# Performance work log

Measured on AMD Instinct MI355X. Metric: run time of the kernel, lower is better.

Reference implementation:

```python
import jax, jax.numpy as jnp
import numpy as np

B, L, D = 2, 256, 256  # batch, length, raw feature dim (W dims are D+1)

def setup_inputs() -> dict:
    key = jax.random.key(0)
    k1, k2, k3, kw = jax.random.split(key, 4)
    layer1 = jax.random.normal(k1, (B, L, D), dtype=jnp.float32)
    layer2 = jax.random.normal(k2, (B, L, D), dtype=jnp.float32)
    layer3 = jax.random.normal(k3, (B, L, D), dtype=jnp.float32)
    # xavier_normal_ for a 3D tensor: fan_in = D+1 * (D+1) receptive? torch treats
    # dim0 as fan_out-ish; we just use a matched-scale gaussian (correctness of the
    # contraction math is what matters for the kernel baseline).
    std = float(np.sqrt(2.0 / ((D + 1) + (D + 1) * (D + 1))))
    W = jax.random.normal(kw, (D + 1, D + 1, D + 1), dtype=jnp.float32) * std
    return {"layer1": layer1, "layer2": layer2, "layer3": layer3, "W": W}

def _append_ones(x):
    ones = jnp.ones(x.shape[:2] + (1,), dtype=x.dtype)
    return jnp.concatenate([x, ones], axis=-1)

def reference(layer1, layer2, layer3, W):
    l1 = _append_ones(layer1)  # [n, L, a]
    l2 = _append_ones(layer2)  # [n, L, b]
    l3 = _append_ones(layer3)  # [n, L, c]
    # Chained contraction: nia,abc -> nibc ; nibc,njb -> nijc ; nijc,nkc -> nijk
    t = jnp.einsum('nia,abc->nibc', l1, W)
    t = jnp.einsum('nibc,njb->nijc', t, l2)
    out = jnp.einsum('nijc,nkc->nijk', t, l3)
    return out
```

## Files before the change

### kernel.cpp

```cpp
#include <hip/hip_runtime.h>

typedef unsigned short u16;
typedef __attribute__((ext_vector_type(8))) short bf16x8;
typedef __attribute__((ext_vector_type(4))) float f32x4;

#define GLOAD_LDS16(gsrc, ldst)                                               \
  __builtin_amdgcn_global_load_lds(                                           \
      (const __attribute__((address_space(1))) void*)(gsrc),                  \
      (__attribute__((address_space(3))) void*)(ldst), 16, 0, 0)

#define LDSOFF(p) \
  ((unsigned)(uintptr_t)(__attribute__((address_space(3))) const void*)(p))

#define SB0 __builtin_amdgcn_sched_barrier(0)

__device__ __forceinline__ u16 f2bf(float x) {
  unsigned u = __float_as_uint(x);
  u = (u + 0x7FFFu + ((u >> 16) & 1u)) >> 16;
  return (u16)u;
}

__global__ void prep_l_kernel(const float* __restrict__ l1,
                              const float* __restrict__ l2,
                              const float* __restrict__ l3,
                              u16* __restrict__ o1, u16* __restrict__ o2,
                              u16* __restrict__ o3) {
  int idx = blockIdx.x * 256 + threadIdx.x;
  const int NR = 512 * 288;
  if (idx >= 3 * NR) return;
  int which = idx / NR, rem = idx - which * NR;
  int r = rem / 288, p = rem - r * 288;
  const float* s = which == 0 ? l1 : which == 1 ? l2 : l3;
  u16* d = which == 0 ? o1 : which == 1 ? o2 : o3;
  float v = (p < 256) ? s[r * 256 + p] : (p == 256 ? 1.0f : 0.0f);
  d[rem] = f2bf(v);
}

__global__ __launch_bounds__(256, 4) void prep_w_kernel(
    const float* __restrict__ W, u16* __restrict__ W2) {
  __shared__ float tf[64][65];
  const int a0 = blockIdx.x * 64, c0 = blockIdx.y * 64, b = blockIdx.z;
  const int t = threadIdx.x;
  const bool bok = (b < 257);

  float v[16];
#pragma unroll
  for (int i = 0; i < 16; ++i) {
    int idx = t + i * 256;
    int ar = idx >> 6, cc = idx & 63;
    int a = a0 + ar, c = c0 + cc;
    v[i] = (bok && a < 257 && c < 257) ? W[((long)a * 257 + b) * 257 + c] : 0.0f;
  }
#pragma unroll
  for (int i = 0; i < 16; ++i) {
    int idx = t + i * 256;
    int ar = idx >> 6, cc = idx & 63;
    tf[cc][ar] = v[i];
  }
  __syncthreads();

#pragma unroll
  for (int p = 0; p < 2; ++p) {
    int q = t + p * 256;
    int cr = q >> 3, ach = q & 7;
    int c = c0 + cr;
    int abase = a0 + ach * 8;
    if (c < 288 && abase < 288) {
      u16 pk[8];
#pragma unroll
      for (int j = 0; j < 8; ++j) pk[j] = f2bf(tf[cr][ach * 8 + j]);
      *(uint4*)(&W2[((long)c * 288 + b) * 288 + abase]) = *(uint4*)pk;
    }
  }
}

__global__ __launch_bounds__(256, 3) void gemm_nt(
    const u16* __restrict__ A, const u16* __restrict__ B, u16* __restrict__ C,
    int K, int lda, int ldb, int ldc) {
  __shared__ u16 As[2][4096];
  __shared__ u16 Bs[2][4096];
  const int t = threadIdx.x;
  const int bid = blockIdx.x;
  const int xcd = bid & 7, s = bid >> 3;
  const int nt = xcd * 77 + (s >> 2);
  const int mt = s & 3;
  const int m0 = mt * 128, n0 = nt * 128;
  const int lane = t & 63;
  const int w = t >> 6;
  const int wr = (w >> 1) * 64, wc = (w & 1) * 64;
  const int r16 = lane & 15;
  const int cgrp = lane >> 4;
  const int rr = cgrp * 4;
  const unsigned ABase = LDSOFF(&As[0][0]);
  const unsigned BBase = LDSOFF(&Bs[0][0]);
  (void)K;

  const u16* PA = A + (long)m0 * lda;
  const u16* PB = B + (long)n0 * ldb;

#define STG(buf, k0)                                                          \
  {                                                                           \
    _Pragma("unroll") for (int _p = 0; _p < 2; ++_p) {                        \
      int _q = t + _p * 256;                                                  \
      int _r = _q >> 2, _g = (_q & 3) ^ ((_r >> 1) & 3);                      \
      GLOAD_LDS16(PA + (long)_r * lda + (k0) + _g * 8, &As[buf][_q * 8]);     \
      GLOAD_LDS16(PB + (long)_r * ldb + (k0) + _g * 8, &Bs[buf][_q * 8]);     \
    }                                                                         \
  }

  f32x4 acc[4][4];
  const f32x4 zero = {0.f, 0.f, 0.f, 0.f};
#pragma unroll
  for (int i = 0; i < 4; ++i)
#pragma unroll
    for (int j = 0; j < 4; ++j) acc[i][j] = zero;

  STG(0, 0);

#define GCOL(NI)                                                              \
  __builtin_amdgcn_s_setprio(1);                                              \
  _Pragma("unroll") for (int _mi = 0; _mi < 4; ++_mi)                         \
    acc[_mi][NI] = __builtin_amdgcn_mfma_f32_16x16x32_bf16(                   \
        af[_mi], bf[NI], acc[_mi][NI], 0, 0, 0);                              \
  __builtin_amdgcn_s_setprio(0);                                              \
  SB0;

#define GSTEP(KS)                                                             \
  {                                                                           \
    asm volatile("s_waitcnt vmcnt(0)" ::: "memory");                          \
    SB0;                                                                      \
    __builtin_amdgcn_s_barrier();                                             \
    SB0;                                                                      \
    bf16x8 af[4], bf[4];                                                      \
    _Pragma("unroll") for (int mi = 0; mi < 4; ++mi) {                        \
      int R = wr + mi * 16 + r16;                                             \
      unsigned ao = ABase + (unsigned)(((((KS) & 1) * 4096) + R * 32 +        \
                                       ((cgrp ^ ((R >> 1) & 3)) * 8)) * 2);   \
      asm volatile("ds_read_b128 %0, %1" : "=v"(af[mi]) : "v"(ao));           \
    }                                                                         \
    _Pragma("unroll") for (int ni = 0; ni < 4; ++ni) {                        \
      int R = wc + ni * 16 + r16;                                             \
      unsigned ao = BBase + (unsigned)(((((KS) & 1) * 4096) + R * 32 +        \
                                       ((cgrp ^ ((R >> 1) & 3)) * 8)) * 2);   \
      asm volatile("ds_read_b128 %0, %1" : "=v"(bf[ni]) : "v"(ao));           \
    }                                                                         \
    SB0;                                                                      \
    if ((KS) < 8) STG(((KS) + 1) & 1, ((KS) + 1) * 32);                       \
    SB0;                                                                      \
    asm volatile("s_waitcnt lgkmcnt(3)" ::: "memory"); SB0;                   \
    GCOL(0)                                                                   \
    asm volatile("s_waitcnt lgkmcnt(2)" ::: "memory"); SB0;                   \
    GCOL(1)                                                                   \
    asm volatile("s_waitcnt lgkmcnt(1)" ::: "memory"); SB0;                   \
    GCOL(2)                                                                   \
    asm volatile("s_waitcnt lgkmcnt(0)" ::: "memory"); SB0;                   \
    GCOL(3)                                                                   \
  }

  GSTEP(0) GSTEP(1) GSTEP(2) GSTEP(3) GSTEP(4)
  GSTEP(5) GSTEP(6) GSTEP(7) GSTEP(8)
#undef GSTEP
#undef GCOL
#undef STG

#pragma unroll
  for (int mi = 0; mi < 4; ++mi) {
    int gm = m0 + wr + mi * 16 + rr;
#pragma unroll
    for (int ni = 0; ni < 4; ++ni) {
      int gc = n0 + wc + ni * 16 + r16;
#pragma unroll
      for (int r = 0; r < 4; ++r)
        C[(long)(gm + r) * ldc + gc] = f2bf(acc[mi][ni][r]);
    }
  }
}

__global__ __launch_bounds__(512, 4) void fused23(
    const u16* __restrict__ l2b, const u16* __restrict__ l3b,
    const u16* __restrict__ T1, float* __restrict__ out) {
  __shared__ u16 S[64 * 280];
  __shared__ u16 Bst[2][8704];
  const int t = threadIdx.x;
  const int lane = t & 63;
  const int w = t >> 6;

  const int bid = blockIdx.x;
  const int xcd = bid & 7;
  const int seq = bid >> 3;
  const int ni = xcd * 64 + (seq >> 2);
  const int q = seq & 3;
  const int n = ni >> 8;

  const int r16 = lane & 15;
  const int cgrp = lane >> 4;
  const int kb = cgrp * 8;
  const int rr = cgrp * 4;
  const f32x4 zero = {0.f, 0.f, 0.f, 0.f};

  const u16* A2 = l2b + (long)n * 73728 + (long)(q * 64) * 288;
  const u16* BT = T1 + (long)ni * 82944;
  const u16* B3 = l3b + (long)n * 73728;
  const unsigned BOF = LDSOFF(&Bst[0][0]);
  const unsigned SOF = LDSOFF(&S[0]);

#define ISSUE_A(buf, kk)                                                      \
  {                                                                           \
    int _q1 = w * 136 + lane;                                                 \
    int _r1 = _q1 >> 2, _g1 = (_q1 & 3) ^ ((_r1 >> 1) & 3);                   \
    GLOAD_LDS16(BT + (long)_r1 * 288 + (kk) * 32 + _g1 * 8,                   \
                &Bst[(buf)][_q1 * 8]);                                        \
    int _q2 = _q1 + 64;                                                       \
    int _r2 = _q2 >> 2, _g2 = (_q2 & 3) ^ ((_r2 >> 1) & 3);                   \
    GLOAD_LDS16(BT + (long)_r2 * 288 + (kk) * 32 + _g2 * 8,                   \
                &Bst[(buf)][_q2 * 8]);                                        \
    if (lane < 8) {                                                           \
      int _q3 = w * 136 + 128 + lane;                                         \
      int _r3 = _q3 >> 2, _g3 = (_q3 & 3) ^ ((_r3 >> 1) & 3);                 \
      GLOAD_LDS16(BT + (long)_r3 * 288 + (kk) * 32 + _g3 * 8,                 \
                  &Bst[(buf)][_q3 * 8]);                                      \
    }                                                                         \
  }
#define ISSUE_B(buf, kk)                                                      \
  {                                                                           \
    _Pragma("unroll") for (int _p = 0; _p < 2; ++_p) {                        \
      int _q = w * 128 + lane + _p * 64;                                      \
      int _r = _q >> 2, _g = (_q & 3) ^ ((_r >> 1) & 3);                      \
      GLOAD_LDS16(B3 + (long)_r * 288 + (kk) * 32 + _g * 8,                   \
                  &Bst[(buf)][_q * 8]);                                       \
    }                                                                         \
  }

  {
    const int wjA = w & 1, wcA = w >> 1;
    const int NT = (wcA == 3) ? 5 : 4;
    f32x4 acc[2][5];
#pragma unroll
    for (int i = 0; i < 2; ++i)
#pragma unroll
      for (int j = 0; j < 5; ++j) acc[i][j] = zero;

    const u16* Ap = A2 + (long)(wjA * 32 + r16) * 288 + kb;
    bf16x8 afc0 = *(const bf16x8*)(Ap);
    bf16x8 afc1 = *(const bf16x8*)(Ap + 16 * 288);
    bf16x8 afn0, afn1;
    SB0;
    ISSUE_A(0, 0) SB0;
    ISSUE_A(1, 1) SB0;

#define FA_STEP(K)                                                            \
  {                                                                           \
    asm volatile("s_waitcnt vmcnt(0)" ::: "memory");                          \
    SB0;                                                                      \
    __builtin_amdgcn_s_barrier();                                             \
    SB0;                                                                      \
    bf16x8 bf[5];                                                             \
    _Pragma("unroll") for (int i = 0; i < 5; ++i) if (i < NT) {               \
      const int R = wcA * 64 + i * 16 + r16;                                  \
      unsigned ao = BOF + (unsigned)((((K) & 1) * 8704 + R * 32 +             \
                                      ((cgrp ^ ((R >> 1) & 3)) * 8)) * 2);    \
      asm volatile("ds_read_b128 %0, %1" : "=v"(bf[i]) : "v"(ao));            \
    }                                                                         \
    SB0;                                                                      \
    if ((K) < 8) {                                                            \
      ISSUE_A(((K) + 1) & 1, (K) + 1);                                        \
      afn0 = *(const bf16x8*)(Ap + ((K) + 1) * 32);                           \
      afn1 = *(const bf16x8*)(Ap + 16 * 288 + ((K) + 1) * 32);                \
    }                                                                         \
    SB0;                                                                      \
    asm volatile("s_waitcnt lgkmcnt(0)" ::: "memory");                        \
    SB0;                                                                      \
    __builtin_amdgcn_s_setprio(1);                                            \
    _Pragma("unroll") for (int i = 0; i < 5; ++i) if (i < NT) {               \
      acc[0][i] = __builtin_amdgcn_mfma_f32_16x16x32_bf16(                    \
          afc0, bf[i], acc[0][i], 0, 0, 0);                                   \
      acc[1][i] = __builtin_amdgcn_mfma_f32_16x16x32_bf16(                    \
          afc1, bf[i], acc[1][i], 0, 0, 0);                                   \
    }                                                                         \
    __builtin_amdgcn_s_setprio(0);                                            \
    SB0;                                                                      \
    afc0 = afn0; afc1 = afn1;                                                 \
  }
    FA_STEP(0) FA_STEP(1) FA_STEP(2) FA_STEP(3) FA_STEP(4)
    FA_STEP(5) FA_STEP(6) FA_STEP(7) FA_STEP(8)
#undef FA_STEP

    __syncthreads();
    ISSUE_B(0, 0);
#pragma unroll
    for (int i = 0; i < 5; ++i) if (i < NT)
#pragma unroll
      for (int mi = 0; mi < 2; ++mi)
#pragma unroll
        for (int qq = 0; qq < 4; ++qq)
          S[(wjA * 32 + mi * 16 + rr + qq) * 280 + wcA * 64 + i * 16 + r16] =
              f2bf(acc[mi][i][qq]);
  }
  __syncthreads();

  {
    const int wjb = w & 1, wk = w >> 1;
    f32x4 acc[2][4];
#pragma unroll
    for (int i = 0; i < 2; ++i)
#pragma unroll
      for (int j = 0; j < 4; ++j) acc[i][j] = zero;

#define FB_MM(NI)                                                             \
  __builtin_amdgcn_s_setprio(1);                                              \
  acc[0][NI] = __builtin_amdgcn_mfma_f32_16x16x32_bf16(af[0], bf[NI], acc[0][NI], 0, 0, 0); \
  acc[1][NI] = __builtin_amdgcn_mfma_f32_16x16x32_bf16(af[1], bf[NI], acc[1][NI], 0, 0, 0); \
  __builtin_amdgcn_s_setprio(0);                                              \
  SB0;

#define FB_STEP(K)                                                            \
  {                                                                           \
    asm volatile("s_waitcnt vmcnt(0)" ::: "memory");                          \
    SB0;                                                                      \
    __builtin_amdgcn_s_barrier();                                             \
    SB0;                                                                      \
    bf16x8 af[2], bf[4];                                                      \
    _Pragma("unroll") for (int mi = 0; mi < 2; ++mi) {                        \
      unsigned ao = SOF + (unsigned)(((wjb * 32 + mi * 16 + r16) * 280 +      \
                                      (K) * 32 + kb) * 2);                    \
      asm volatile("ds_read_b128 %0, %1" : "=v"(af[mi]) : "v"(ao));           \
    }                                                                         \
    _Pragma("unroll") for (int nj = 0; nj < 4; ++nj) {                        \
      const int R = wk * 64 + nj * 16 + r16;                                  \
      unsigned ao = BOF + (unsigned)((((K) & 1) * 8704 + R * 32 +             \
                                      ((cgrp ^ ((R >> 1) & 3)) * 8)) * 2);    \
      asm volatile("ds_read_b128 %0, %1" : "=v"(bf[nj]) : "v"(ao));           \
    }                                                                         \
    SB0;                                                                      \
    if ((K) < 7) ISSUE_B(((K) + 1) & 1, (K) + 1);                             \
    SB0;                                                                      \
    asm volatile("s_waitcnt lgkmcnt(3)" ::: "memory"); SB0;                   \
    FB_MM(0)                                                                  \
    asm volatile("s_waitcnt lgkmcnt(2)" ::: "memory"); SB0;                   \
    FB_MM(1)                                                                  \
    asm volatile("s_waitcnt lgkmcnt(1)" ::: "memory"); SB0;                   \
    FB_MM(2)                                                                  \
    asm volatile("s_waitcnt lgkmcnt(0)" ::: "memory"); SB0;                   \
    FB_MM(3)                                                                  \
  }
    FB_STEP(0) FB_STEP(1) FB_STEP(2) FB_STEP(3)
    FB_STEP(4) FB_STEP(5) FB_STEP(6) FB_STEP(7)
#undef FB_STEP
#undef FB_MM

    float s256[2][4];
#pragma unroll
    for (int mi = 0; mi < 2; ++mi)
#pragma unroll
      for (int qq = 0; qq < 4; ++qq)
        s256[mi][qq] = __uint_as_float(
            (unsigned)S[(wjb * 32 + mi * 16 + rr + qq) * 280 + 256] << 16);

    float* O = out + (long)ni * 65536 + (long)(q * 64 + wjb * 32) * 256 + wk * 64;
#pragma unroll
    for (int mi = 0; mi < 2; ++mi)
#pragma unroll
      for (int nj = 0; nj < 4; ++nj)
#pragma unroll
        for (int qq = 0; qq < 4; ++qq)
          O[(long)(mi * 16 + rr + qq) * 256 + nj * 16 + r16] =
              acc[mi][nj][qq] + s256[mi][qq];
  }
#undef ISSUE_A
#undef ISSUE_B
}

extern "C" void kernel_launch(void* const* d_in, const int* in_sizes, int n_in,
                              void* d_out, int out_size, void* d_ws, size_t ws_size,
                              hipStream_t stream) {
  const float* l1 = (const float*)d_in[0];
  const float* l2 = (const float*)d_in[1];
  const float* l3 = (const float*)d_in[2];
  const float* W = (const float*)d_in[3];
  float* out = (float*)d_out;
  char* ws = (char*)d_ws;

  const long LB = 512L * 288 * 2;
  u16* l1b = (u16*)ws;
  u16* l2b = (u16*)(ws + LB);
  u16* l3b = (u16*)(ws + 2 * LB);
  u16* T1 = (u16*)(ws + 3 * LB);
  u16* W2 = (u16*)d_out;

  prep_l_kernel<<<1728, 256, 0, stream>>>(l1, l2, l3, l1b, l2b, l3b);

  dim3 gw(5, 5, 288);
  prep_w_kernel<<<gw, 256, 0, stream>>>(W, W2);

  gemm_nt<<<2464, 256, 0, stream>>>(l1b, W2, T1, 288, 288, 288, 82944);

  fused23<<<2048, 512, 0, stream>>>(l2b, l3b, T1, out);
}
```

Measured before the change: 147.8 us.

## Halve fused23 row tile to 32 rows and double grid for occupancy

Each fused23 block now handles 32 rows of j instead of 64, so the grid doubles to 4096 blocks and the S scratch buffer shrinks. Launch bounds rise to 6 blocks per CU, with fewer accumulators per wave. The goal is higher occupancy and better latency hiding. The cost is that each block reloads the full T1 and l3 B tiles while doing half the MFMA work, which doubles global and LDS traffic per unit of compute.

```diff
diff --git a/kernel.cpp b/kernel.cpp
--- a/kernel.cpp
+++ b/kernel.cpp
@@ -176,10 +176,10 @@
   }
 }
 
-__global__ __launch_bounds__(512, 4) void fused23(
+__global__ __launch_bounds__(512, 6) void fused23(
     const u16* __restrict__ l2b, const u16* __restrict__ l3b,
     const u16* __restrict__ T1, float* __restrict__ out) {
-  __shared__ u16 S[64 * 280];
+  __shared__ u16 S[32 * 280];
   __shared__ u16 Bst[2][8704];
   const int t = threadIdx.x;
   const int lane = t & 63;
@@ -188,8 +188,8 @@
   const int bid = blockIdx.x;
   const int xcd = bid & 7;
   const int seq = bid >> 3;
-  const int ni = xcd * 64 + (seq >> 2);
-  const int q = seq & 3;
+  const int ni = xcd * 64 + (seq >> 3);
+  const int sub = seq & 7;
   const int n = ni >> 8;
 
   const int r16 = lane & 15;
@@ -198,7 +198,7 @@
   const int rr = cgrp * 4;
   const f32x4 zero = {0.f, 0.f, 0.f, 0.f};
 
-  const u16* A2 = l2b + (long)n * 73728 + (long)(q * 64) * 288;
+  const u16* A2 = l2b + (long)n * 73728 + (long)(sub * 32) * 288;
   const u16* BT = T1 + (long)ni * 82944;
   const u16* B3 = l3b + (long)n * 73728;
   const unsigned BOF = LDSOFF(&Bst[0][0]);
@@ -234,16 +234,13 @@
   {
     const int wjA = w & 1, wcA = w >> 1;
     const int NT = (wcA == 3) ? 5 : 4;
-    f32x4 acc[2][5];
-#pragma unroll
-    for (int i = 0; i < 2; ++i)
-#pragma unroll
-      for (int j = 0; j < 5; ++j) acc[i][j] = zero;
-
-    const u16* Ap = A2 + (long)(wjA * 32 + r16) * 288 + kb;
-    bf16x8 afc0 = *(const bf16x8*)(Ap);
-    bf16x8 afc1 = *(const bf16x8*)(Ap + 16 * 288);
-    bf16x8 afn0, afn1;
+    f32x4 acc[5];
+#pragma unroll
+    for (int j = 0; j < 5; ++j) acc[j] = zero;
+
+    const u16* Ap = A2 + (long)(wjA * 16 + r16) * 288 + kb;
+    bf16x8 afc = *(const bf16x8*)(Ap);
+    bf16x8 afn;
     SB0;
     ISSUE_A(0, 0) SB0;
     ISSUE_A(1, 1) SB0;
@@ -264,22 +261,18 @@
     SB0;                                                                      \
     if ((K) < 8) {                                                            \
       ISSUE_A(((K) + 1) & 1, (K) + 1);                                        \
-      afn0 = *(const bf16x8*)(Ap + ((K) + 1) * 32);                           \
-      afn1 = *(const bf16x8*)(Ap + 16 * 288 + ((K) + 1) * 32);                \
+      afn = *(const bf16x8*)(Ap + ((K) + 1) * 32);                            \
     }                                                                         \
     SB0;                                                                      \
     asm volatile("s_waitcnt lgkmcnt(0)" ::: "memory");                        \
     SB0;                                                                      \
     __builtin_amdgcn_s_setprio(1);                                            \
-    _Pragma("unroll") for (int i = 0; i < 5; ++i) if (i < NT) {               \
-      acc[0][i] = __builtin_amdgcn_mfma_f32_16x16x32_bf16(                    \
-          afc0, bf[i], acc[0][i], 0, 0, 0);                                   \
-      acc[1][i] = __builtin_amdgcn_mfma_f32_16x16x32_bf16(                    \
-          afc1, bf[i], acc[1][i], 0, 0, 0);                                   \
-    }                                                                         \
+    _Pragma("unroll") for (int i = 0; i < 5; ++i) if (i < NT)                 \
+      acc[i] = __builtin_amdgcn_mfma_f32_16x16x32_bf16(                       \
+          afc, bf[i], acc[i], 0, 0, 0);                                       \
     __builtin_amdgcn_s_setprio(0);                                            \
     SB0;                                                                      \
-    afc0 = afn0; afc1 = afn1;                                                 \
+    afc = afn;                                                                \
   }
     FA_STEP(0) FA_STEP(1) FA_STEP(2) FA_STEP(3) FA_STEP(4)
     FA_STEP(5) FA_STEP(6) FA_STEP(7) FA_STEP(8)
@@ -290,26 +283,21 @@
 #pragma unroll
     for (int i = 0; i < 5; ++i) if (i < NT)
 #pragma unroll
-      for (int mi = 0; mi < 2; ++mi)
-#pragma unroll
-        for (int qq = 0; qq < 4; ++qq)
-          S[(wjA * 32 + mi * 16 + rr + qq) * 280 + wcA * 64 + i * 16 + r16] =
-              f2bf(acc[mi][i][qq]);
+      for (int qq = 0; qq < 4; ++qq)
+        S[(wjA * 16 + rr + qq) * 280 + wcA * 64 + i * 16 + r16] =
+            f2bf(acc[i][qq]);
   }
   __syncthreads();
 
   {
     const int wjb = w & 1, wk = w >> 1;
-    f32x4 acc[2][4];
-#pragma unroll
-    for (int i = 0; i < 2; ++i)
-#pragma unroll
-      for (int j = 0; j < 4; ++j) acc[i][j] = zero;
+    f32x4 acc[4];
+#pragma unroll
+    for (int j = 0; j < 4; ++j) acc[j] = zero;
 
 #define FB_MM(NI)                                                             \
   __builtin_amdgcn_s_setprio(1);                                              \
-  acc[0][NI] = __builtin_amdgcn_mfma_f32_16x16x32_bf16(af[0], bf[NI], acc[0][NI], 0, 0, 0); \
-  acc[1][NI] = __builtin_amdgcn_mfma_f32_16x16x32_bf16(af[1], bf[NI], acc[1][NI], 0, 0, 0); \
+  acc[NI] = __builtin_amdgcn_mfma_f32_16x16x32_bf16(af0, bf[NI], acc[NI], 0, 0, 0); \
   __builtin_amdgcn_s_setprio(0);                                              \
   SB0;
 
@@ -319,11 +307,11 @@
     SB0;                                                                      \
     __builtin_amdgcn_s_barrier();                                             \
     SB0;                                                                      \
-    bf16x8 af[2], bf[4];                                                      \
-    _Pragma("unroll") for (int mi = 0; mi < 2; ++mi) {                        \
-      unsigned ao = SOF + (unsigned)(((wjb * 32 + mi * 16 + r16) * 280 +      \
+    bf16x8 af0, bf[4];                                                        \
+    {                                                                         \
+      unsigned ao = SOF + (unsigned)(((wjb * 16 + r16) * 280 +                \
                                       (K) * 32 + kb) * 2);                    \
-      asm volatile("ds_read_b128 %0, %1" : "=v"(af[mi]) : "v"(ao));           \
+      asm volatile("ds_read_b128 %0, %1" : "=v"(af0) : "v"(ao));              \
     }                                                                         \
     _Pragma("unroll") for (int nj = 0; nj < 4; ++nj) {                        \
       const int R = wk * 64 + nj * 16 + r16;                                  \
@@ -348,23 +336,18 @@
 #undef FB_STEP
 #undef FB_MM
 
-    float s256[2][4];
-#pragma unroll
-    for (int mi = 0; mi < 2; ++mi)
+    float s256[4];
+#pragma unroll
+    for (int qq = 0; qq < 4; ++qq)
+      s256[qq] = __uint_as_float(
+          (unsigned)S[(wjb * 16 + rr + qq) * 280 + 256] << 16);
+
+    float* O = out + (long)ni * 65536 + (long)(sub * 32 + wjb * 16) * 256 + wk * 64;
+#pragma unroll
+    for (int nj = 0; nj < 4; ++nj)
 #pragma unroll
       for (int qq = 0; qq < 4; ++qq)
-        s256[mi][qq] = __uint_as_float(
-            (unsigned)S[(wjb * 32 + mi * 16 + rr + qq) * 280 + 256] << 16);
-
-    float* O = out + (long)ni * 65536 + (long)(q * 64 + wjb * 32) * 256 + wk * 64;
-#pragma unroll
-    for (int mi = 0; mi < 2; ++mi)
-#pragma unroll
-      for (int nj = 0; nj < 4; ++nj)
-#pragma unroll
-        for (int qq = 0; qq < 4; ++qq)
-          O[(long)(mi * 16 + rr + qq) * 256 + nj * 16 + r16] =
-              acc[mi][nj][qq] + s256[mi][qq];
+        O[(long)(rr + qq) * 256 + nj * 16 + r16] = acc[nj][qq] + s256[qq];
   }
 #undef ISSUE_A
 #undef ISSUE_B
@@ -394,5 +377,5 @@
 
   gemm_nt<<<2464, 256, 0, stream>>>(l1b, W2, T1, 288, 288, 288, 82944);
 
-  fused23<<<2048, 512, 0, stream>>>(l2b, l3b, T1, out);
-}
+  fused23<<<4096, 512, 0, stream>>>(l2b, l3b, T1, out);
+}
```

After: 169.5 us. 14.7% more time.
